# Kernel tuning notes

Hardware: AMD Instinct MI355X
Metric: run time of the kernel (lower is better)

Reference implementation:

```python
import jax, jax.numpy as jnp
import numpy as np

EPS = 1e-5
HEADS = 4
N_SIDE = 32  # im_h == im_w


def _rel_pos_indices(n):
    idx = np.arange(n)
    xi = np.repeat(idx, n)
    yi = np.tile(idx, n)
    pos = np.stack([xi, yi])                      # [2, n^2]
    d = pos[:, None, :] - pos[:, :, None]          # [2, n^2, n^2]
    d = np.clip(d, -n, n) + (n - 1)
    return d[0], d[1]


def _conv1x1(x, W):
    # x: [b,c,H,W], W: [o,c]
    return jnp.einsum('bchw,oc->bohw', x, W)


def _bn(x, g, b, m, v):
    inv = jax.lax.rsqrt(v + EPS)
    return (x - m[:, None, None]) * (inv * g)[:, None, None] + b[:, None, None]


def setup_inputs() -> dict:
    key = jax.random.key(0)
    ks = jax.random.split(key, 8)
    b, dim, H = 16, 256, N_SIDE
    dim_k, heads, dim_out = 16, HEADS, 256
    dim_v = dim_out // heads
    return {
        'x': jax.random.normal(ks[0], (b, dim, H, H), jnp.float32),
        'Wq': jax.random.normal(ks[1], (dim_k * heads, dim), jnp.float32) * 0.05,
        'Wk': jax.random.normal(ks[2], (dim_k, dim), jnp.float32) * 0.05,
        'Wv': jax.random.normal(ks[3], (dim_v, dim), jnp.float32) * 0.05,
        'gq': jnp.ones((dim_k * heads,), jnp.float32),
        'bq': jnp.zeros((dim_k * heads,), jnp.float32),
        'mq': jax.random.normal(ks[4], (dim_k * heads,), jnp.float32) * 0.1,
        'vq': jax.random.uniform(ks[5], (dim_k * heads,), jnp.float32, 0.5, 1.5),
        'gv': jnp.ones((dim_v,), jnp.float32),
        'bv': jnp.zeros((dim_v,), jnp.float32),
        'mv': jax.random.normal(ks[6], (dim_v,), jnp.float32) * 0.1,
        'vv': jax.random.uniform(ks[7], (dim_v,), jnp.float32, 0.5, 1.5),
        'rel_pos_emb': jax.random.normal(jax.random.fold_in(key, 7), (2 * H - 1, 2 * H - 1, dim_k), jnp.float32) * 0.05,
    }


def reference(x, Wq, Wk, Wv, gq, bq, mq, vq, gv, bv, mv, vv, rel_pos_emb):
    b, c, H, W = x.shape
    heads = HEADS
    m = H * W
    dim_k = Wk.shape[0]
    dim_v = Wv.shape[0]

    Q = _bn(_conv1x1(x, Wq), gq, bq, mq, vq)              # [b, h*k, H, W]
    K = _conv1x1(x, Wk)                                   # [b, k, H, W]
    V = _bn(_conv1x1(x, Wv), gv, bv, mv, vv)              # [b, v, H, W]

    Q = Q.reshape(b, heads, dim_k, m).transpose(0, 1, 3, 2)   # [b, h, m, k]
    K = K.reshape(b, dim_k, m).transpose(0, 2, 1)             # [b, m, k]
    V = V.reshape(b, dim_v, m).transpose(0, 2, 1)             # [b, m, v]

    sK = jax.nn.softmax(K, axis=-1)  # NOTE: source softmaxes over k, not m
    lam_c = jnp.einsum('bmk,bmv->bkv', sK, V)
    content = jnp.einsum('bhnk,bkv->bnhv', Q, lam_c)

    r0, r1 = _rel_pos_indices(H)
    emb = rel_pos_emb[r0, r1]                         # [m, m, k]
    lam_p = jnp.einsum('nmk,bmv->bnkv', emb, V)       # [b, m, k, v]
    position = jnp.einsum('bhnk,bnkv->bnhv', Q, lam_p)

    out = content + position                          # [b, m, h, v]
    return out.reshape(b, H, W, heads * dim_v)
```

## Files before the change

### kernel.cpp

```cpp
#include <hip/hip_runtime.h>
#include <math.h>

namespace {
typedef unsigned short u16;
typedef __attribute__((ext_vector_type(4))) float f32x4;
typedef __attribute__((ext_vector_type(8))) short bf16x8;

constexpr int kB  = 16;
constexpr int kC  = 256;
constexpr int kM  = 1024;

__device__ inline u16 f2b(float f) {
    union { float f; unsigned u; } un; un.f = f;
    unsigned r = un.u + 0x7FFF + ((un.u >> 16) & 1);
    return (u16)(r >> 16);
}
__device__ inline float b2f(u16 u) {
    union { unsigned u; float f; } un; un.u = ((unsigned)u) << 16; return un.f;
}

__global__ __launch_bounds__(256) void k_prep(
    const float* __restrict__ Wq, const float* __restrict__ Wk,
    const float* __restrict__ Wv,
    const float* __restrict__ gq, const float* __restrict__ bq,
    const float* __restrict__ mq, const float* __restrict__ vq,
    const float* __restrict__ gv, const float* __restrict__ bv,
    const float* __restrict__ mv, const float* __restrict__ vv,
    const float* __restrict__ rpe,
    u16* __restrict__ Wb, float* __restrict__ bb, u16* __restrict__ rpe_b)
{
    const int bid = blockIdx.x;
    const int t = threadIdx.x;
    if (bid < 9) {
        const int oc = bid * 16 + (t >> 4);
        const int c0 = (t & 15) * 16;
        float s, bias;
        const float* wrow;
        if (oc < 64)      { float inv = rsqrtf(vq[oc] + 1e-5f); s = inv * gq[oc]; bias = bq[oc] - mq[oc] * s; wrow = Wq + (size_t)oc * kC; }
        else if (oc < 80) { s = 1.f; bias = 0.f; wrow = Wk + (size_t)(oc - 64) * kC; }
        else              { int i2 = oc - 80; float inv = rsqrtf(vv[i2] + 1e-5f); s = inv * gv[i2]; bias = bv[i2] - mv[i2] * s; wrow = Wv + (size_t)i2 * kC; }
#pragma unroll
        for (int cc = 0; cc < 16; ++cc)
            Wb[(size_t)oc * kC + c0 + cc] = f2b(wrow[c0 + cc] * s);
        if (c0 == 0) bb[oc] = bias;
    } else {
        const int dr = bid - 9;
        for (int e = t; e < 2048; e += 256) {
            int dc = e >> 5, k = e & 31;
            float v = (dc < 63 && k < 16) ? rpe[((size_t)dr * 63 + dc) * 16 + k] : 0.f;
            rpe_b[((size_t)dr * 64 + dc) * 32 + k] = f2b(v);
        }
    }
}

__global__ __launch_bounds__(256) void k_qkv(
    const float* __restrict__ x, const u16* __restrict__ Wb,
    const float* __restrict__ bb,
    u16* __restrict__ Qb, float* __restrict__ Kf, u16* __restrict__ Vb)
{
    __shared__ float Xs[256][36];

    const int b  = blockIdx.y;
    const int m0 = blockIdx.x * 32;
    const int t  = threadIdx.x;
    const int w  = t >> 6, lane = t & 63, li = lane & 15, lg = lane >> 4;
    const int mh = w & 1, tg = w >> 1;
    const int mw = mh * 16;

#pragma unroll
    for (int j = 0; j < 8; ++j) {
        int e = t + 256 * j;
        int c = e >> 3, m4 = (e & 7) * 4;
        *(float4*)&Xs[c][m4] = *(const float4*)&x[(size_t)(b * kC + c) * kM + m0 + m4];
    }
    __syncthreads();

    const int m = m0 + mw + li;

    if (tg == 0) {
        f32x4 acc[5];
#pragma unroll
        for (int i = 0; i < 5; ++i) acc[i] = (f32x4){0.f, 0.f, 0.f, 0.f};
#pragma unroll 2
        for (int ch = 0; ch < 8; ++ch) {
            const int c0 = ch * 32 + lg * 8;
            bf16x8 bfr;
#pragma unroll
            for (int j = 0; j < 8; ++j) bfr[j] = (short)f2b(Xs[c0 + j][mw + li]);
#pragma unroll
            for (int i = 0; i < 5; ++i) {
                bf16x8 afr = *(const bf16x8*)&Wb[(size_t)(i * 16 + li) * kC + c0];
                acc[i] = __builtin_amdgcn_mfma_f32_16x16x32_bf16(afr, bfr, acc[i], 0, 0, 0);
            }
        }
#pragma unroll
        for (int i = 0; i < 5; ++i) {
            const int ocb = i * 16 + lg * 4;
            float o[4];
#pragma unroll
            for (int reg = 0; reg < 4; ++reg) o[reg] = acc[i][reg] + bb[ocb + reg];
            if (i < 4) {
                u16 pk[4];
#pragma unroll
                for (int reg = 0; reg < 4; ++reg) pk[reg] = f2b(o[reg]);
                u16* qp = Qb + ((size_t)(b * 4 + i) * kM + m) * 32;
                *(uint2*)&qp[lg * 4] = *(const uint2*)pk;
                uint2 z; z.x = 0u; z.y = 0u;
                *(uint2*)&qp[16 + lg * 4] = z;
            } else {
#pragma unroll
                for (int reg = 0; reg < 4; ++reg)
                    Kf[(size_t)(b * 16 + lg * 4 + reg) * kM + m] = o[reg];
            }
        }
    } else {
        f32x4 acc[4];
#pragma unroll
        for (int i = 0; i < 4; ++i) acc[i] = (f32x4){0.f, 0.f, 0.f, 0.f};
#pragma unroll 2
        for (int ch = 0; ch < 8; ++ch) {
            const int c0 = ch * 32 + lg * 8;
            bf16x8 bfr;
#pragma unroll
            for (int j = 0; j < 8; ++j) bfr[j] = (short)f2b(Xs[c0 + j][mw + li]);
#pragma unroll
            for (int i = 0; i < 4; ++i) {
                bf16x8 afr = *(const bf16x8*)&Wb[(size_t)((5 + i) * 16 + li) * kC + c0];
                acc[i] = __builtin_amdgcn_mfma_f32_16x16x32_bf16(afr, bfr, acc[i], 0, 0, 0);
            }
        }
#pragma unroll
        for (int i = 0; i < 4; ++i) {
            const int ocb = (5 + i) * 16 + lg * 4;
            const int vb = i * 16 + lg * 4;
#pragma unroll
            for (int reg = 0; reg < 4; ++reg) {
                float o = acc[i][reg] + bb[ocb + reg];
                Vb[(size_t)(b * 64 + vb + reg) * kM + m] = f2b(o);
            }
        }
    }
}

__global__ __launch_bounds__(256) void k_lam(
    const float* __restrict__ Kf, const u16* __restrict__ Vb,
    float* __restrict__ lam_parts)
{
    __shared__ float Ks[16][64];
    __shared__ float Vsh[64][69];

    const int b = blockIdx.y, mb = blockIdx.x;
    const int m0 = mb * 64;
    const int t = threadIdx.x;
    const float* Kc = Kf + (size_t)b * 16 * kM + m0;
    const u16*   Vc = Vb + (size_t)b * 64 * kM + m0;

#pragma unroll
    for (int j = 0; j < 4; ++j) {
        int e = t + 256 * j;
        Ks[e >> 6][e & 63] = Kc[(size_t)(e >> 6) * kM + (e & 63)];
    }
#pragma unroll
    for (int j = 0; j < 4; ++j) {
        int e = t + 256 * j;
        int v = e >> 4, mq = (e & 15) * 4;
        uint2 pv = *(const uint2*)&Vc[(size_t)v * kM + mq];
        u16 pp[4]; *(uint2*)pp = pv;
#pragma unroll
        for (int i = 0; i < 4; ++i) Vsh[v][mq + i] = b2f(pp[i]);
    }
    __syncthreads();

    if (t < 64) {
        float vals[16];
        float mx = -1e30f;
#pragma unroll
        for (int k = 0; k < 16; ++k) { vals[k] = Ks[k][t]; mx = fmaxf(mx, vals[k]); }
        float sum = 0.f;
#pragma unroll
        for (int k = 0; k < 16; ++k) { vals[k] = __expf(vals[k] - mx); sum += vals[k]; }
        const float inv = 1.f / sum;
#pragma unroll
        for (int k = 0; k < 16; ++k) Ks[k][t] = vals[k] * inv;
    }
    __syncthreads();

    const int v = t & 63, kq = t >> 6;
    float a[4] = {0.f, 0.f, 0.f, 0.f};
#pragma unroll 4
    for (int mm = 0; mm < 64; ++mm) {
        const float vv_ = Vsh[v][mm];
#pragma unroll
        for (int j = 0; j < 4; ++j) a[j] += Ks[kq * 4 + j][mm] * vv_;
    }
    float* o = lam_parts + (size_t)(mb * kB + b) * 1024;
#pragma unroll
    for (int j = 0; j < 4; ++j) o[(kq * 4 + j) * 64 + v] = a[j];
}

__global__ __launch_bounds__(256) void k_attn(
    const u16* __restrict__ Qb, const u16* __restrict__ Vb,
    const u16* __restrict__ rpe_b, const float* __restrict__ lam_parts,
    float* __restrict__ out)
{
    __shared__ u16 Rl[128][40];
    __shared__ u16 Vls[64][72];
    __shared__ u16 Sl[4][32][72];
    __shared__ float lc[16][65];

    const int b = blockIdx.y, nrow = blockIdx.x, n0 = nrow * 32;
    const int t = threadIdx.x;
    const int h = t >> 6, lane = t & 63, li = lane & 15, lg = lane >> 4;
    const u16* Vbb = Vb + (size_t)b * 64 * kM;
    u16* Sh = &Sl[h][0][0];

    for (int e = t; e < 1024; e += 256) {
        float s = 0.f;
#pragma unroll
        for (int p = 0; p < 16; ++p) s += lam_parts[(size_t)(p * kB + b) * 1024 + e];
        lc[e >> 6][e & 63] = s;
    }

    const u16* Qbase = Qb + ((size_t)(b * 4 + h) * kM + n0) * 32;
    bf16x8 qf[2];
    qf[0] = *(const bf16x8*)&Qbase[(size_t)li * 32 + lg * 8];
    qf[1] = *(const bf16x8*)&Qbase[(size_t)(16 + li) * 32 + lg * 8];

    bf16x8 rpre[2], vpre[2];
#pragma unroll
    for (int ii = 0; ii < 2; ++ii) {
        int s = 2 * t + ii;
        int rrow = s >> 2, rkc = (s & 3) * 8;
        int dr = (rrow >> 6) - nrow + 31;
        rpre[ii] = *(const bf16x8*)&rpe_b[((size_t)dr * 64 + (rrow & 63)) * 32 + rkc];
        int v = s >> 3, mc = (s & 7) * 8;
        vpre[ii] = *(const bf16x8*)&Vbb[(size_t)v * kM + mc];
    }

    __syncthreads();

    f32x4 acc[2][4];
#pragma unroll
    for (int c = 0; c < 4; ++c) {
        bf16x8 cb;
#pragma unroll
        for (int j = 0; j < 8; ++j) {
            int k = lg * 8 + j;
            cb[j] = (k < 16) ? (short)f2b(lc[k][16 * c + li]) : (short)0;
        }
        f32x4 z = {0.f, 0.f, 0.f, 0.f};
        acc[0][c] = __builtin_amdgcn_mfma_f32_16x16x32_bf16(qf[0], cb, z, 0, 0, 0);
        acc[1][c] = __builtin_amdgcn_mfma_f32_16x16x32_bf16(qf[1], cb, z, 0, 0, 0);
    }

    for (int it = 0; it < 16; ++it) {
        __syncthreads();
#pragma unroll
        for (int ii = 0; ii < 2; ++ii) {
            int s = 2 * t + ii;
            *(bf16x8*)&Rl[s >> 2][(s & 3) * 8] = rpre[ii];
            *(bf16x8*)&Vls[s >> 3][(s & 7) * 8] = vpre[ii];
        }
        __syncthreads();
        if (it < 15) {
            const int itn = it + 1;
#pragma unroll
            for (int ii = 0; ii < 2; ++ii) {
                int s = 2 * t + ii;
                int rrow = s >> 2, rkc = (s & 3) * 8;
                int dr = 2 * itn + (rrow >> 6) - nrow + 31;
                rpre[ii] = *(const bf16x8*)&rpe_b[((size_t)dr * 64 + (rrow & 63)) * 32 + rkc];
                int v = s >> 3, mc = (s & 7) * 8;
                vpre[ii] = *(const bf16x8*)&Vbb[(size_t)v * kM + itn * 64 + mc];
            }
        }

#pragma unroll
        for (int mi = 0; mi < 2; ++mi) {
            f32x4 tq[4][2];
#pragma unroll
            for (int g = 0; g < 4; ++g) {
                bf16x8 ra = *(const bf16x8*)&Rl[mi * 64 + 16 * g + li][lg * 8];
                f32x4 z = {0.f, 0.f, 0.f, 0.f};
                tq[g][0] = __builtin_amdgcn_mfma_f32_16x16x32_bf16(ra, qf[0], z, 0, 0, 0);
                tq[g][1] = __builtin_amdgcn_mfma_f32_16x16x32_bf16(ra, qf[1], z, 0, 0, 0);
            }
#pragma unroll
            for (int g = 0; g < 4; ++g)
#pragma unroll
                for (int r = 0; r < 2; ++r) {
                    const int nl = 16 * r + li;
                    const int dcb = 16 * g + 4 * lg;
#pragma unroll
                    for (int reg = 0; reg < 4; ++reg) {
                        const int ml = dcb + reg + nl - 31;
                        if ((unsigned)ml < 32u)
                            Sh[nl * 72 + mi * 32 + ml] = f2b(tq[g][r][reg]);
                    }
                }

            bf16x8 vfc[4];
#pragma unroll
            for (int c = 0; c < 4; ++c)
                vfc[c] = *(const bf16x8*)&Vls[16 * c + li][mi * 32 + lg * 8];
#pragma unroll
            for (int r = 0; r < 2; ++r) {
                bf16x8 sa = *(const bf16x8*)&Sh[(size_t)(16 * r + li) * 72 + mi * 32 + lg * 8];
#pragma unroll
                for (int c = 0; c < 4; ++c)
                    acc[r][c] = __builtin_amdgcn_mfma_f32_16x16x32_bf16(sa, vfc[c], acc[r][c], 0, 0, 0);
            }
        }
    }

    float* ob = out + ((size_t)b * kM + n0) * 256 + h * 64;
#pragma unroll
    for (int r = 0; r < 2; ++r)
#pragma unroll
        for (int c = 0; c < 4; ++c)
#pragma unroll
            for (int reg = 0; reg < 4; ++reg)
                ob[(size_t)(16 * r + 4 * lg + reg) * 256 + 16 * c + li] = acc[r][c][reg];
}

}

extern "C" void kernel_launch(void* const* d_in, const int* in_sizes, int n_in,
                              void* d_out, int out_size, void* d_ws, size_t ws_size,
                              hipStream_t stream) {
    const float* x   = (const float*)d_in[0];
    const float* Wq  = (const float*)d_in[1];
    const float* Wk  = (const float*)d_in[2];
    const float* Wv  = (const float*)d_in[3];
    const float* gq  = (const float*)d_in[4];
    const float* bq  = (const float*)d_in[5];
    const float* mq  = (const float*)d_in[6];
    const float* vq  = (const float*)d_in[7];
    const float* gv  = (const float*)d_in[8];
    const float* bv  = (const float*)d_in[9];
    const float* mv  = (const float*)d_in[10];
    const float* vv  = (const float*)d_in[11];
    const float* rpe = (const float*)d_in[12];
    float* out = (float*)d_out;

    float* Kf        = (float*)d_ws;
    float* lam_parts = Kf + (size_t)16 * 16 * 1024;
    float* bbuf      = lam_parts + (size_t)16 * 16 * 1024;
    u16*   Qb        = (u16*)(bbuf + 256);
    u16*   Vb        = Qb + (size_t)16 * 4 * 1024 * 32;
    u16*   rpe_b     = Vb + (size_t)16 * 64 * 1024;
    u16*   Wb        = rpe_b + (size_t)63 * 64 * 32;

    k_prep<<<72, 256, 0, stream>>>(Wq, Wk, Wv, gq, bq, mq, vq, gv, bv, mv, vv,
                                   rpe, Wb, bbuf, rpe_b);
    k_qkv<<<dim3(32, 16), 256, 0, stream>>>(x, Wb, bbuf, Qb, Kf, Vb);
    k_lam<<<dim3(16, 16), 256, 0, stream>>>(Kf, Vb, lam_parts);
    k_attn<<<dim3(32, 16), 256, 0, stream>>>(Qb, Vb, rpe_b, lam_parts, out);
}
```

Baseline: 158.3 us.

## Halve attention query tile, skip zero relative-position tiles, stream V from global

The attention kernel now handles 16 query positions per block instead of 32, so twice as many blocks launch. Per mrow iteration it computes only the three relative-position tiles that can be non-zero, in place of four per half. It reads V and the relative embeddings straight from global memory into registers, dropping the shared-memory staging and its two barriers per iteration. It also adds an occupancy launch bound and MFMA priority hints. The QKV projection is split the same way: 16 positions per block, with the nine output tiles spread unevenly over four waves. The trade-off is more global loads per block and less reuse of rpe and V across queries.

```diff
diff --git a/kernel.cpp b/kernel.cpp
--- a/kernel.cpp
+++ b/kernel.cpp
@@ -58,86 +58,63 @@
     const float* __restrict__ bb,
     u16* __restrict__ Qb, float* __restrict__ Kf, u16* __restrict__ Vb)
 {
-    __shared__ float Xs[256][36];
+    __shared__ float Xs[256][18];
 
     const int b  = blockIdx.y;
-    const int m0 = blockIdx.x * 32;
+    const int m0 = blockIdx.x * 16;
     const int t  = threadIdx.x;
     const int w  = t >> 6, lane = t & 63, li = lane & 15, lg = lane >> 4;
-    const int mh = w & 1, tg = w >> 1;
-    const int mw = mh * 16;
-
-#pragma unroll
-    for (int j = 0; j < 8; ++j) {
+
+#pragma unroll
+    for (int j = 0; j < 4; ++j) {
         int e = t + 256 * j;
-        int c = e >> 3, m4 = (e & 7) * 4;
+        int c = e >> 2, m4 = (e & 3) * 4;
         *(float4*)&Xs[c][m4] = *(const float4*)&x[(size_t)(b * kC + c) * kM + m0 + m4];
     }
     __syncthreads();
 
-    const int m = m0 + mw + li;
-
-    if (tg == 0) {
-        f32x4 acc[5];
-#pragma unroll
-        for (int i = 0; i < 5; ++i) acc[i] = (f32x4){0.f, 0.f, 0.f, 0.f};
-#pragma unroll 2
-        for (int ch = 0; ch < 8; ++ch) {
-            const int c0 = ch * 32 + lg * 8;
-            bf16x8 bfr;
-#pragma unroll
-            for (int j = 0; j < 8; ++j) bfr[j] = (short)f2b(Xs[c0 + j][mw + li]);
-#pragma unroll
-            for (int i = 0; i < 5; ++i) {
-                bf16x8 afr = *(const bf16x8*)&Wb[(size_t)(i * 16 + li) * kC + c0];
-                acc[i] = __builtin_amdgcn_mfma_f32_16x16x32_bf16(afr, bfr, acc[i], 0, 0, 0);
-            }
-        }
-#pragma unroll
-        for (int i = 0; i < 5; ++i) {
-            const int ocb = i * 16 + lg * 4;
-            float o[4];
-#pragma unroll
-            for (int reg = 0; reg < 4; ++reg) o[reg] = acc[i][reg] + bb[ocb + reg];
-            if (i < 4) {
-                u16 pk[4];
-#pragma unroll
-                for (int reg = 0; reg < 4; ++reg) pk[reg] = f2b(o[reg]);
-                u16* qp = Qb + ((size_t)(b * 4 + i) * kM + m) * 32;
-                *(uint2*)&qp[lg * 4] = *(const uint2*)pk;
-                uint2 z; z.x = 0u; z.y = 0u;
-                *(uint2*)&qp[16 + lg * 4] = z;
-            } else {
-#pragma unroll
-                for (int reg = 0; reg < 4; ++reg)
-                    Kf[(size_t)(b * 16 + lg * 4 + reg) * kM + m] = o[reg];
-            }
-        }
-    } else {
-        f32x4 acc[4];
-#pragma unroll
-        for (int i = 0; i < 4; ++i) acc[i] = (f32x4){0.f, 0.f, 0.f, 0.f};
-#pragma unroll 2
-        for (int ch = 0; ch < 8; ++ch) {
-            const int c0 = ch * 32 + lg * 8;
-            bf16x8 bfr;
-#pragma unroll
-            for (int j = 0; j < 8; ++j) bfr[j] = (short)f2b(Xs[c0 + j][mw + li]);
-#pragma unroll
-            for (int i = 0; i < 4; ++i) {
-                bf16x8 afr = *(const bf16x8*)&Wb[(size_t)((5 + i) * 16 + li) * kC + c0];
-                acc[i] = __builtin_amdgcn_mfma_f32_16x16x32_bf16(afr, bfr, acc[i], 0, 0, 0);
-            }
-        }
-#pragma unroll
-        for (int i = 0; i < 4; ++i) {
-            const int ocb = (5 + i) * 16 + lg * 4;
-            const int vb = i * 16 + lg * 4;
-#pragma unroll
-            for (int reg = 0; reg < 4; ++reg) {
-                float o = acc[i][reg] + bb[ocb + reg];
-                Vb[(size_t)(b * 64 + vb + reg) * kM + m] = f2b(o);
-            }
+    const int nt = (w == 0) ? 3 : 2;
+    const int t0 = (w == 0) ? 0 : 2 * w + 1;
+
+    f32x4 acc[3];
+#pragma unroll
+    for (int i = 0; i < 3; ++i) acc[i] = (f32x4){0.f, 0.f, 0.f, 0.f};
+
+    for (int ch = 0; ch < 8; ++ch) {
+        const int c0 = ch * 32 + lg * 8;
+        bf16x8 bfr;
+#pragma unroll
+        for (int j = 0; j < 8; ++j) bfr[j] = (short)f2b(Xs[c0 + j][li]);
+        for (int i = 0; i < nt; ++i) {
+            bf16x8 afr = *(const bf16x8*)&Wb[(size_t)((t0 + i) * 16 + li) * kC + c0];
+            acc[i] = __builtin_amdgcn_mfma_f32_16x16x32_bf16(afr, bfr, acc[i], 0, 0, 0);
+        }
+    }
+
+    const int m = m0 + li;
+    for (int i = 0; i < nt; ++i) {
+        const int tile = t0 + i;
+        const int ocb = tile * 16 + lg * 4;
+        float o[4];
+#pragma unroll
+        for (int reg = 0; reg < 4; ++reg) o[reg] = acc[i][reg] + bb[ocb + reg];
+        if (tile < 4) {
+            u16 pk[4];
+#pragma unroll
+            for (int reg = 0; reg < 4; ++reg) pk[reg] = f2b(o[reg]);
+            u16* qp = Qb + ((size_t)(b * 4 + tile) * kM + m) * 32;
+            *(uint2*)&qp[lg * 4] = *(const uint2*)pk;
+            uint2 z; z.x = 0u; z.y = 0u;
+            *(uint2*)&qp[16 + lg * 4] = z;
+        } else if (tile == 4) {
+#pragma unroll
+            for (int reg = 0; reg < 4; ++reg)
+                Kf[(size_t)(b * 16 + lg * 4 + reg) * kM + m] = o[reg];
+        } else {
+            const int vb = (tile - 5) * 16 + lg * 4;
+#pragma unroll
+            for (int reg = 0; reg < 4; ++reg)
+                Vb[(size_t)(b * 64 + vb + reg) * kM + m] = f2b(o[reg]);
         }
     }
 }
@@ -198,19 +175,21 @@
     for (int j = 0; j < 4; ++j) o[(kq * 4 + j) * 64 + v] = a[j];
 }
 
-__global__ __launch_bounds__(256) void k_attn(
+__global__ __launch_bounds__(256, 4) void k_attn(
     const u16* __restrict__ Qb, const u16* __restrict__ Vb,
     const u16* __restrict__ rpe_b, const float* __restrict__ lam_parts,
     float* __restrict__ out)
 {
-    __shared__ u16 Rl[128][40];
-    __shared__ u16 Vls[64][72];
-    __shared__ u16 Sl[4][32][72];
     __shared__ float lc[16][65];
-
-    const int b = blockIdx.y, nrow = blockIdx.x, n0 = nrow * 32;
+    __shared__ u16 Sl[4][16][68];
+
+    const int b = blockIdx.y, nblk = blockIdx.x, n0 = nblk * 16;
     const int t = threadIdx.x;
     const int h = t >> 6, lane = t & 63, li = lane & 15, lg = lane >> 4;
+    const int ny = n0 >> 5;
+    const int dshift = 31 - (n0 & 16);
+    const int gbase = (n0 & 16) ? 0 : 1;
+
     const u16* Vbb = Vb + (size_t)b * 64 * kM;
     u16* Sh = &Sl[h][0][0];
 
@@ -222,24 +201,19 @@
     }
 
     const u16* Qbase = Qb + ((size_t)(b * 4 + h) * kM + n0) * 32;
-    bf16x8 qf[2];
-    qf[0] = *(const bf16x8*)&Qbase[(size_t)li * 32 + lg * 8];
-    qf[1] = *(const bf16x8*)&Qbase[(size_t)(16 + li) * 32 + lg * 8];
-
-    bf16x8 rpre[2], vpre[2];
-#pragma unroll
-    for (int ii = 0; ii < 2; ++ii) {
-        int s = 2 * t + ii;
-        int rrow = s >> 2, rkc = (s & 3) * 8;
-        int dr = (rrow >> 6) - nrow + 31;
-        rpre[ii] = *(const bf16x8*)&rpe_b[((size_t)dr * 64 + (rrow & 63)) * 32 + rkc];
-        int v = s >> 3, mc = (s & 7) * 8;
-        vpre[ii] = *(const bf16x8*)&Vbb[(size_t)v * kM + mc];
+    bf16x8 qf = *(const bf16x8*)&Qbase[(size_t)li * 32 + lg * 8];
+
+    bf16x8 ra[3];
+    {
+        const int dr = 31 - ny;
+#pragma unroll
+        for (int g = 0; g < 3; ++g)
+            ra[g] = *(const bf16x8*)&rpe_b[((size_t)dr * 64 + (gbase + g) * 16 + li) * 32 + lg * 8];
     }
 
     __syncthreads();
 
-    f32x4 acc[2][4];
+    f32x4 acc[4];
 #pragma unroll
     for (int c = 0; c < 4; ++c) {
         bf16x8 cb;
@@ -249,78 +223,61 @@
             cb[j] = (k < 16) ? (short)f2b(lc[k][16 * c + li]) : (short)0;
         }
         f32x4 z = {0.f, 0.f, 0.f, 0.f};
-        acc[0][c] = __builtin_amdgcn_mfma_f32_16x16x32_bf16(qf[0], cb, z, 0, 0, 0);
-        acc[1][c] = __builtin_amdgcn_mfma_f32_16x16x32_bf16(qf[1], cb, z, 0, 0, 0);
-    }
-
-    for (int it = 0; it < 16; ++it) {
-        __syncthreads();
-#pragma unroll
-        for (int ii = 0; ii < 2; ++ii) {
-            int s = 2 * t + ii;
-            *(bf16x8*)&Rl[s >> 2][(s & 3) * 8] = rpre[ii];
-            *(bf16x8*)&Vls[s >> 3][(s & 7) * 8] = vpre[ii];
-        }
-        __syncthreads();
-        if (it < 15) {
-            const int itn = it + 1;
-#pragma unroll
-            for (int ii = 0; ii < 2; ++ii) {
-                int s = 2 * t + ii;
-                int rrow = s >> 2, rkc = (s & 3) * 8;
-                int dr = 2 * itn + (rrow >> 6) - nrow + 31;
-                rpre[ii] = *(const bf16x8*)&rpe_b[((size_t)dr * 64 + (rrow & 63)) * 32 + rkc];
-                int v = s >> 3, mc = (s & 7) * 8;
-                vpre[ii] = *(const bf16x8*)&Vbb[(size_t)v * kM + itn * 64 + mc];
-            }
-        }
-
-#pragma unroll
-        for (int mi = 0; mi < 2; ++mi) {
-            f32x4 tq[4][2];
-#pragma unroll
-            for (int g = 0; g < 4; ++g) {
-                bf16x8 ra = *(const bf16x8*)&Rl[mi * 64 + 16 * g + li][lg * 8];
-                f32x4 z = {0.f, 0.f, 0.f, 0.f};
-                tq[g][0] = __builtin_amdgcn_mfma_f32_16x16x32_bf16(ra, qf[0], z, 0, 0, 0);
-                tq[g][1] = __builtin_amdgcn_mfma_f32_16x16x32_bf16(ra, qf[1], z, 0, 0, 0);
-            }
-#pragma unroll
-            for (int g = 0; g < 4; ++g)
-#pragma unroll
-                for (int r = 0; r < 2; ++r) {
-                    const int nl = 16 * r + li;
-                    const int dcb = 16 * g + 4 * lg;
-#pragma unroll
-                    for (int reg = 0; reg < 4; ++reg) {
-                        const int ml = dcb + reg + nl - 31;
-                        if ((unsigned)ml < 32u)
-                            Sh[nl * 72 + mi * 32 + ml] = f2b(tq[g][r][reg]);
-                    }
-                }
-
-            bf16x8 vfc[4];
-#pragma unroll
-            for (int c = 0; c < 4; ++c)
-                vfc[c] = *(const bf16x8*)&Vls[16 * c + li][mi * 32 + lg * 8];
-#pragma unroll
-            for (int r = 0; r < 2; ++r) {
-                bf16x8 sa = *(const bf16x8*)&Sh[(size_t)(16 * r + li) * 72 + mi * 32 + lg * 8];
-#pragma unroll
-                for (int c = 0; c < 4; ++c)
-                    acc[r][c] = __builtin_amdgcn_mfma_f32_16x16x32_bf16(sa, vfc[c], acc[r][c], 0, 0, 0);
-            }
-        }
+        acc[c] = __builtin_amdgcn_mfma_f32_16x16x32_bf16(qf, cb, z, 0, 0, 0);
+    }
+
+    const int swr = li * 68;
+    const int src0 = swr + 8 * lg + dshift - li;
+
+#pragma unroll 2
+    for (int mrow = 0; mrow < 32; ++mrow) {
+        bf16x8 vf[4];
+#pragma unroll
+        for (int c = 0; c < 4; ++c)
+            vf[c] = *(const bf16x8*)&Vbb[(size_t)(16 * c + li) * kM + mrow * 32 + lg * 8];
+
+        f32x4 tq[3];
+#pragma unroll
+        for (int g = 0; g < 3; ++g) {
+            f32x4 z = {0.f, 0.f, 0.f, 0.f};
+            tq[g] = __builtin_amdgcn_mfma_f32_16x16x32_bf16(ra[g], qf, z, 0, 0, 0);
+        }
+
+        if (mrow < 31) {
+            const int dr = mrow + 1 - ny + 31;
+#pragma unroll
+            for (int g = 0; g < 3; ++g)
+                ra[g] = *(const bf16x8*)&rpe_b[((size_t)dr * 64 + (gbase + g) * 16 + li) * 32 + lg * 8];
+        }
+
+#pragma unroll
+        for (int g = 0; g < 3; ++g) {
+            u16 pk[4];
+#pragma unroll
+            for (int reg = 0; reg < 4; ++reg) pk[reg] = f2b(tq[g][reg]);
+            *(uint2*)&Sh[swr + (gbase + g) * 16 + 4 * lg] = *(const uint2*)pk;
+        }
+
+        asm volatile("" ::: "memory");
+
+        bf16x8 sa;
+#pragma unroll
+        for (int j = 0; j < 8; ++j)
+            sa[j] = (short)Sh[src0 + j];
+
+        __builtin_amdgcn_s_setprio(1);
+#pragma unroll
+        for (int c = 0; c < 4; ++c)
+            acc[c] = __builtin_amdgcn_mfma_f32_16x16x32_bf16(sa, vf[c], acc[c], 0, 0, 0);
+        __builtin_amdgcn_s_setprio(0);
     }
 
     float* ob = out + ((size_t)b * kM + n0) * 256 + h * 64;
 #pragma unroll
-    for (int r = 0; r < 2; ++r)
-#pragma unroll
-        for (int c = 0; c < 4; ++c)
-#pragma unroll
-            for (int reg = 0; reg < 4; ++reg)
-                ob[(size_t)(16 * r + 4 * lg + reg) * 256 + 16 * c + li] = acc[r][c][reg];
+    for (int c = 0; c < 4; ++c)
+#pragma unroll
+        for (int reg = 0; reg < 4; ++reg)
+            ob[(size_t)(4 * lg + reg) * 256 + 16 * c + li] = acc[c][reg];
 }
 
 }
@@ -353,7 +310,7 @@
 
     k_prep<<<72, 256, 0, stream>>>(Wq, Wk, Wv, gq, bq, mq, vq, gv, bv, mv, vv,
                                    rpe, Wb, bbuf, rpe_b);
-    k_qkv<<<dim3(32, 16), 256, 0, stream>>>(x, Wb, bbuf, Qb, Kf, Vb);
+    k_qkv<<<dim3(64, 16), 256, 0, stream>>>(x, Wb, bbuf, Qb, Kf, Vb);
     k_lam<<<dim3(16, 16), 256, 0, stream>>>(Kf, Vb, lam_parts);
-    k_attn<<<dim3(32, 16), 256, 0, stream>>>(Qb, Vb, rpe_b, lam_parts, out);
-}
+    k_attn<<<dim3(64, 16), 256, 0, stream>>>(Qb, Vb, rpe_b, lam_parts, out);
+}
```

Result: slower. 193.5 us (+22.2%).
